# Kernel optimization log

Hardware: AMD Instinct MI355X
Metric: run time of the kernel (lower is better)

Reference implementation:

```python
import jax, jax.numpy as jnp
import numpy as np

EPS = 1e-7  # keras.backend.epsilon()
ROUTINGS = 3


def squash(v, axis=-1):
    # scale = ||v||^2 / (1+||v||^2) / sqrt(||v||^2 + eps)
    s2 = jnp.sum(jnp.square(v), axis=axis, keepdims=True)
    return v * (s2 / (1.0 + s2) / jnp.sqrt(s2 + EPS))


def setup_inputs() -> dict:
    key = jax.random.key(0)
    k1, k2 = jax.random.split(key)
    B, I, P = 256, 1152, 8   # batch, primcap_num, primcap_dim
    J, D = 10, 16            # digitcap_num, digitcap_dim
    x = jax.random.normal(k1, (B, I, P), dtype=jnp.float32)
    W = jax.random.normal(k2, (I, J, D, P), dtype=jnp.float32) * 0.01
    return {"x": x, "W": W}


def reference(x, W):
    # votes u_hat[b,i,j,d] = W[i,j,d,:] @ x[b,i,:]  (implicit broadcast, no tiling)
    votes = jnp.einsum('ijdp,bip->bijd', W, x)            # [B,I,J,D]
    B, I, J, _ = votes.shape
    b = jnp.zeros((B, I, J), dtype=votes.dtype)
    v = None
    for r in range(ROUTINGS):
        c = jax.nn.softmax(b, axis=2)                      # over digit capsules
        s = jnp.einsum('bij,bijd->bjd', c, votes)          # weighted sum over prim caps
        v = squash(s, axis=-1)                             # [B,J,D]
        if r < ROUTINGS - 1:
            b = b + jnp.einsum('bijd,bjd->bij', votes, v)  # agreement
    return v
```

## Files before the change

kernel.cpp:

```cpp
#include <hip/hip_runtime.h>
#include <cstdint>
#include <cstddef>

constexpr int Bn = 256, In = 1152, Pn = 8, Jn = 10, Dn = 16;
constexpr int CA = 4, NCH = In / CA;
constexpr int PADX = 9;

typedef float v2f __attribute__((ext_vector_type(2)));

template <int CTRL>
__device__ __forceinline__ float dpp_add(float v) {
  const int s =
      __builtin_amdgcn_update_dpp(0, __float_as_int(v), CTRL, 0xf, 0xf, true);
  return v + __int_as_float(s);
}

__device__ __forceinline__ float rowsum16(float v) {
  v = dpp_add<0xB1>(v);
  v = dpp_add<0x4E>(v);
  v = dpp_add<0x124>(v);
  v = dpp_add<0x128>(v);
  return v;
}

__device__ __forceinline__ v2f pkdot8(const float4 w0, const float4 w1,
                                      const float4 x0, const float4 x1) {
  v2f wa, wb, wc, wd, xa, xb, xc, xd;
  wa.x = w0.x; wa.y = w0.y; wb.x = w0.z; wb.y = w0.w;
  wc.x = w1.x; wc.y = w1.y; wd.x = w1.z; wd.y = w1.w;
  xa.x = x0.x; xa.y = x0.y; xb.x = x0.z; xb.y = x0.w;
  xc.x = x1.x; xc.y = x1.y; xd.x = x1.z; xd.y = x1.w;
  v2f acc = wa * xa;
  acc = __builtin_elementwise_fma(wb, xb, acc);
  acc = __builtin_elementwise_fma(wc, xc, acc);
  acc = __builtin_elementwise_fma(wd, xd, acc);
  return acc;
}

template <int MODE>
__global__ __launch_bounds__(256)
__attribute__((amdgpu_waves_per_eu(3, 4)))
void capsV(const float* __restrict__ x, const float* __restrict__ w,
           const float* __restrict__ vsumT, float* __restrict__ spart) {
  __shared__ float4 wlds[CA * Jn * 2 * 16];
  __shared__ float4 xlds[32 * PADX];
  const int t = threadIdx.x;
  const int d = t & 15, q = t >> 4;
  const int ch = blockIdx.x;
  const int bbase = blockIdx.y * 32;
  const int b0 = bbase + q, b1 = b0 + 16;
  const int i0 = ch * CA;

  {
    const float4* wg =
        reinterpret_cast<const float4*>(w + (size_t)i0 * (Jn * Dn * Pn));
    for (int k = 0; k < 5; ++k) {
      const int g = t + k * 256;
      const int h = g & 1, dd = (g >> 1) & 15, ij = g >> 5;
      wlds[(ij * 2 + h) * 16 + dd] = wg[g];
    }
  }
  {
    const int bl = t >> 3, idx = t & 7;
    xlds[bl * PADX + idx] = reinterpret_cast<const float4*>(
        x + ((size_t)(bbase + bl) * In + i0) * Pn)[idx];
  }

  v2f vs2[Jn], acc2[Jn];
  #pragma unroll
  for (int j = 0; j < Jn; ++j) {
    acc2[j] = (v2f)(0.f);
    if (MODE) {
      vs2[j].x = vsumT[((size_t)j * Bn + b0) * Dn + d];
      vs2[j].y = vsumT[((size_t)j * Bn + b1) * Dn + d];
    }
  }

  __syncthreads();

  for (int ii = 0; ii < CA; ++ii) {
    const float4 xa0 = xlds[q * PADX + ii * 2];
    const float4 xa1 = xlds[q * PADX + ii * 2 + 1];
    const float4 xb0 = xlds[(q + 16) * PADX + ii * 2];
    const float4 xb1 = xlds[(q + 16) * PADX + ii * 2 + 1];

    v2f vt2[Jn];
    #pragma unroll
    for (int j = 0; j < Jn; ++j) {
      const float4* wrow = &wlds[((ii * Jn + j) * 2) * 16 + d];
      const float4 w0 = wrow[0];
      const float4 w1 = wrow[16];
      const v2f pa = pkdot8(w0, w1, xa0, xa1);
      const v2f pb = pkdot8(w0, w1, xb0, xb1);
      vt2[j].x = pa.x + pa.y;
      vt2[j].y = pb.x + pb.y;
    }

    if (MODE) {
      v2f e2[Jn], sum2 = (v2f)(0.f);
      #pragma unroll
      for (int j = 0; j < Jn; ++j) {
        const v2f lp = vt2[j] * vs2[j];
        e2[j].x = __expf(rowsum16(lp.x));
        e2[j].y = __expf(rowsum16(lp.y));
        sum2 += e2[j];
      }
      v2f inv2;
      inv2.x = __builtin_amdgcn_rcpf(sum2.x);
      inv2.y = __builtin_amdgcn_rcpf(sum2.y);
      #pragma unroll
      for (int j = 0; j < Jn; ++j)
        acc2[j] = __builtin_elementwise_fma(e2[j] * inv2, vt2[j], acc2[j]);
    } else {
      #pragma unroll
      for (int j = 0; j < Jn; ++j) acc2[j] += vt2[j];
    }
  }

  const float cs = MODE ? 1.f : 0.1f;
  #pragma unroll
  for (int j = 0; j < Jn; ++j) {
    spart[(((size_t)ch * Jn + j) * Bn + b0) * Dn + d] = acc2[j].x * cs;
    spart[(((size_t)ch * Jn + j) * Bn + b1) * Dn + d] = acc2[j].y * cs;
  }
}

template <int MODE>
__global__ __launch_bounds__(1024) void capsF(
    const float* __restrict__ spart, float* __restrict__ vsumT,
    float* __restrict__ out) {
  __shared__ float red[8][8][16];
  const int t = threadIdx.x;
  const int cg = t >> 7, r = t & 127, g = r >> 4, d = r & 15;
  const int j = blockIdx.x, b = blockIdx.y * 8 + g;

  const size_t cstride = (size_t)Jn * Bn * Dn;
  const size_t cstep = 8 * cstride;
  const float* sp = spart + (((size_t)cg * Jn + j) * Bn + b) * Dn + d;
  float s0 = 0.f, s1 = 0.f;
  #pragma unroll 4
  for (int k = 0; k < NCH / 8; k += 2) {
    s0 += sp[0];
    s1 += sp[cstep];
    sp += 2 * cstep;
  }
  red[cg][g][d] = s0 + s1;
  __syncthreads();
  if (t < 128) {
    float z = 0.f;
    #pragma unroll
    for (int c = 0; c < 8; ++c) z += red[c][g][d];
    const float n2 = rowsum16(z * z);
    const float sc = n2 / (1.f + n2) / sqrtf(n2 + 1e-7f);
    const float v = z * sc;
    if (MODE == 2) {
      out[((size_t)b * Jn + j) * Dn + d] = v;
    } else if (MODE == 1) {
      vsumT[((size_t)j * Bn + b) * Dn + d] += v;
    } else {
      vsumT[((size_t)j * Bn + b) * Dn + d] = v;
    }
  }
}

extern "C" void kernel_launch(void* const* d_in, const int* in_sizes, int n_in,
                              void* d_out, int out_size, void* d_ws, size_t ws_size,
                              hipStream_t stream) {
  const float* x = (const float*)d_in[0];
  const float* w = (const float*)d_in[1];
  float* vsumT = (float*)d_ws;
  float* spart = vsumT + (size_t)Jn * Bn * Dn;
  float* out = (float*)d_out;

  const dim3 gV(NCH, Bn / 32), gF(Jn, Bn / 8);

  capsV<0><<<gV, 256, 0, stream>>>(x, w, nullptr, spart);
  capsF<0><<<gF, 1024, 0, stream>>>(spart, vsumT, out);

  capsV<1><<<gV, 256, 0, stream>>>(x, w, vsumT, spart);
  capsF<1><<<gF, 1024, 0, stream>>>(spart, vsumT, out);

  capsV<1><<<gV, 256, 0, stream>>>(x, w, vsumT, spart);
  capsF<2><<<gF, 1024, 0, stream>>>(spart, vsumT, out);
}
```

Before: 158.3 us.

## Replace per-chunk partial sums with global atomic accumulation and lighter squash kernel

The vote kernel now atomically adds its per-chunk weighted sums into a single [J,B,D] buffer instead of writing a full per-chunk partial array. The finishing kernel becomes a simple per-element squash that also zeroes the buffer for the next routing pass, and a memset clears it up front. This removes the large write and read-back of partial sums across all chunks. In exchange it adds atomic contention on the same addresses from many blocks and makes float summation order nondeterministic.

Result: slower. 333.1 us (+110.4%).

```diff
diff --git a/kernel.cpp b/kernel.cpp
--- a/kernel.cpp
+++ b/kernel.cpp
@@ -41,7 +41,7 @@
 __global__ __launch_bounds__(256)
 __attribute__((amdgpu_waves_per_eu(3, 4)))
 void capsV(const float* __restrict__ x, const float* __restrict__ w,
-           const float* __restrict__ vsumT, float* __restrict__ spart) {
+           const float* __restrict__ vsumT, float* __restrict__ sglob) {
   __shared__ float4 wlds[CA * Jn * 2 * 16];
   __shared__ float4 xlds[32 * PADX];
   const int t = threadIdx.x;
@@ -120,46 +120,31 @@
   const float cs = MODE ? 1.f : 0.1f;
   #pragma unroll
   for (int j = 0; j < Jn; ++j) {
-    spart[(((size_t)ch * Jn + j) * Bn + b0) * Dn + d] = acc2[j].x * cs;
-    spart[(((size_t)ch * Jn + j) * Bn + b1) * Dn + d] = acc2[j].y * cs;
+    unsafeAtomicAdd(&sglob[((size_t)j * Bn + b0) * Dn + d], acc2[j].x * cs);
+    unsafeAtomicAdd(&sglob[((size_t)j * Bn + b1) * Dn + d], acc2[j].y * cs);
   }
 }
 
 template <int MODE>
-__global__ __launch_bounds__(1024) void capsF(
-    const float* __restrict__ spart, float* __restrict__ vsumT,
+__global__ __launch_bounds__(256) void capsFsq(
+    float* __restrict__ sglob, float* __restrict__ vsumT,
     float* __restrict__ out) {
-  __shared__ float red[8][8][16];
   const int t = threadIdx.x;
-  const int cg = t >> 7, r = t & 127, g = r >> 4, d = r & 15;
-  const int j = blockIdx.x, b = blockIdx.y * 8 + g;
+  const int d = t & 15, g = t >> 4;
+  const int j = blockIdx.x, b = blockIdx.y * 16 + g;
 
-  const size_t cstride = (size_t)Jn * Bn * Dn;
-  const size_t cstep = 8 * cstride;
-  const float* sp = spart + (((size_t)cg * Jn + j) * Bn + b) * Dn + d;
-  float s0 = 0.f, s1 = 0.f;
-  #pragma unroll 4
-  for (int k = 0; k < NCH / 8; k += 2) {
-    s0 += sp[0];
-    s1 += sp[cstep];
-    sp += 2 * cstep;
-  }
-  red[cg][g][d] = s0 + s1;
-  __syncthreads();
-  if (t < 128) {
-    float z = 0.f;
-    #pragma unroll
-    for (int c = 0; c < 8; ++c) z += red[c][g][d];
-    const float n2 = rowsum16(z * z);
-    const float sc = n2 / (1.f + n2) / sqrtf(n2 + 1e-7f);
-    const float v = z * sc;
-    if (MODE == 2) {
-      out[((size_t)b * Jn + j) * Dn + d] = v;
-    } else if (MODE == 1) {
-      vsumT[((size_t)j * Bn + b) * Dn + d] += v;
-    } else {
-      vsumT[((size_t)j * Bn + b) * Dn + d] = v;
-    }
+  const size_t idx = ((size_t)j * Bn + b) * Dn + d;
+  const float z = sglob[idx];
+  const float n2 = rowsum16(z * z);
+  const float sc = n2 / (1.f + n2) / sqrtf(n2 + 1e-7f);
+  const float v = z * sc;
+  sglob[idx] = 0.f;
+  if (MODE == 2) {
+    out[((size_t)b * Jn + j) * Dn + d] = v;
+  } else if (MODE == 1) {
+    vsumT[idx] += v;
+  } else {
+    vsumT[idx] = v;
   }
 }
 
@@ -169,17 +154,19 @@
   const float* x = (const float*)d_in[0];
   const float* w = (const float*)d_in[1];
   float* vsumT = (float*)d_ws;
-  float* spart = vsumT + (size_t)Jn * Bn * Dn;
+  float* sglob = vsumT + (size_t)Jn * Bn * Dn;
   float* out = (float*)d_out;
 
-  const dim3 gV(NCH, Bn / 32), gF(Jn, Bn / 8);
+  hipMemsetAsync(sglob, 0, (size_t)Jn * Bn * Dn * sizeof(float), stream);
 
-  capsV<0><<<gV, 256, 0, stream>>>(x, w, nullptr, spart);
-  capsF<0><<<gF, 1024, 0, stream>>>(spart, vsumT, out);
+  const dim3 gV(NCH, Bn / 32), gF(Jn, Bn / 16);
 
-  capsV<1><<<gV, 256, 0, stream>>>(x, w, vsumT, spart);
-  capsF<1><<<gF, 1024, 0, stream>>>(spart, vsumT, out);
+  capsV<0><<<gV, 256, 0, stream>>>(x, w, nullptr, sglob);
+  capsFsq<0><<<gF, 256, 0, stream>>>(sglob, vsumT, out);
 
-  capsV<1><<<gV, 256, 0, stream>>>(x, w, vsumT, spart);
-  capsF<2><<<gF, 1024, 0, stream>>>(spart, vsumT, out);
+  capsV<1><<<gV, 256, 0, stream>>>(x, w, vsumT, sglob);
+  capsFsq<1><<<gF, 256, 0, stream>>>(sglob, vsumT, out);
+
+  capsV<1><<<gV, 256, 0, stream>>>(x, w, vsumT, sglob);
+  capsFsq<2><<<gF, 256, 0, stream>>>(sglob, vsumT, out);
 }
```
